# Kernel optimization log

Hardware: AMD Instinct MI355X
Metric: run time of the kernel (lower is better)

Reference implementation:

```python
import jax, jax.numpy as jnp
import numpy as np

# dims: batch, query/key grid HxW, channels, heads (== W for the final matmul to be consistent)
B, H, W, DIM, HEADS = 4, 64, 64, 512, 64
QKV = DIM // HEADS          # per-head projection width (8)
SCALE = QKV ** -0.5         # self.qkv_dim ** -0.5


def setup_inputs() -> dict:
    key = jax.random.key(0)
    k1, k2, k3, k4 = jax.random.split(key, 4)
    x = jax.random.normal(k1, (B, H, W, DIM), dtype=jnp.float32)
    # AttnVector weights, init std=0.01 as in nn.init.normal_(self.w, std=0.01)
    w_q = jax.random.normal(k2, (DIM, HEADS, QKV), dtype=jnp.float32) * 0.01
    w_k = jax.random.normal(k3, (DIM, HEADS, QKV), dtype=jnp.float32) * 0.01
    w_v = jax.random.normal(k4, (DIM, HEADS, QKV), dtype=jnp.float32) * 0.01
    return {"x": x, "w_q": w_q, "w_k": w_k, "w_v": w_v}


def reference(x, w_q, w_k, w_v):
    # q, k, v projections: einsum 'bhwc,cnp->bhwnp' -> [B,H,W,HEADS,QKV]
    q = jnp.einsum('bhwc,cnp->bhwnp', x, w_q)
    k = jnp.einsum('bhwc,cnp->bhwnp', x, w_k)
    v = jnp.einsum('bhwc,cnp->bhwnp', x, w_v)
    # Literal math of torch.einsum('bhwc,bpqd->bhwpq', q, k): the contracted
    # labels c and d appear only once each, so each tensor is summed over its
    # feature axes independently and the result is an outer product over
    # spatial positions: weights[b,h,w,p,q] = sum(q[b,h,w]) * sum(k[b,p,q]).
    qs = q.sum(axis=(-2, -1))  # [B,H,W]
    ks = k.sum(axis=(-2, -1))  # [B,H,W]
    weights = qs[:, :, :, None, None] * ks[:, None, None, :, :]  # [B,H,W,H,W]
    # dropout (p=0.1) is identity in eval mode; scale applied BEFORE softmax,
    # exactly as in the source (weights *= scale; softmax(dim=-1)).
    weights = jax.nn.softmax(weights * SCALE, axis=-1)
    # weights @ value: batch dims (B,H,W), matmul (H_p, W_q) @ (heads==W_q, QKV)
    attn = jnp.einsum('bhwpq,bhwqd->bhwpd', weights, v)  # [B,H,W,H,QKV]
    return attn
```

## Files before the change

kernel.cpp:

```cpp
#include <hip/hip_runtime.h>
#include <hip/hip_bf16.h>
#include <math.h>


#define SCALE 0.35355339059327373f
#define LOG2E 1.4426950408889634f

typedef __attribute__((ext_vector_type(8))) short s16x8;
typedef __attribute__((ext_vector_type(4))) float f32x4;
typedef __attribute__((ext_vector_type(4))) unsigned int u32x4;

union frag_cast { u32x4 u; s16x8 s; };

__device__ __forceinline__ unsigned short f2bf(float f) {
    unsigned u = __float_as_uint(f);
    u += 0x7FFF + ((u >> 16) & 1);
    return (unsigned short)(u >> 16);
}
__device__ __forceinline__ float bf2f(unsigned short h) {
    return __uint_as_float(((unsigned)h) << 16);
}

__device__ __forceinline__ void gl16(const void* g, void* l) {
    __builtin_amdgcn_global_load_lds(
        (const __attribute__((address_space(1))) unsigned int*)g,
        (__attribute__((address_space(3))) unsigned int*)l, 16, 0, 0);
}

__device__ __forceinline__ void split2(float f0, float f1, unsigned& h, unsigned& l) {
    unsigned u0 = __float_as_uint(f0), u1 = __float_as_uint(f1);
    h = __builtin_amdgcn_perm(u1, u0, 0x07060302u);
    float l0 = f0 - __uint_as_float(u0 & 0xffff0000u);
    float l1 = f1 - __uint_as_float(u1 & 0xffff0000u);
    unsigned lp;
    asm("v_cvt_pk_bf16_f32 %0, %1, %2" : "=v"(lp) : "v"(l0), "v"(l1));
    l = lp;
}

__global__ __launch_bounds__(256) void k_prep(const float* __restrict__ wq,
                                              const float* __restrict__ wk,
                                              const float* __restrict__ wv,
                                              float* __restrict__ wqs,
                                              float* __restrict__ wks,
                                              unsigned short* __restrict__ wh,
                                              unsigned short* __restrict__ wl) {
    __shared__ float tile[64][65];
    if (blockIdx.x >= 64) {
        int gw = ((int)blockIdx.x - 64) * 4 + (threadIdx.x >> 6);
        int lane = threadIdx.x & 63;
        const float* src = (gw < 512) ? wq : wk;
        int c = gw & 511;
        const float4* row = (const float4*)(src + (size_t)c * 512);
        float4 a = row[lane * 2], b = row[lane * 2 + 1];
        float s = a.x + a.y + a.z + a.w + b.x + b.y + b.z + b.w;
#pragma unroll
        for (int off = 32; off; off >>= 1) s += __shfl_xor(s, off);
        if (lane == 0) {
            if (gw < 512) wqs[c] = s; else wks[c] = s;
        }
        return;
    }
    const int ti = (int)blockIdx.x >> 3;
    const int tj = (int)blockIdx.x & 7;
    const int r = threadIdx.x >> 4;
    const int c4 = (threadIdx.x & 15) * 4;
#pragma unroll
    for (int i = 0; i < 4; ++i) {
        int kl = r + i * 16;
        float4 v = *(const float4*)(wv + (size_t)(ti * 64 + kl) * 512 + tj * 64 + c4);
        tile[kl][c4 + 0] = v.x; tile[kl][c4 + 1] = v.y;
        tile[kl][c4 + 2] = v.z; tile[kl][c4 + 3] = v.w;
    }
    __syncthreads();
#pragma unroll
    for (int i = 0; i < 4; ++i) {
        int nl = r + i * 16;
        int n = tj * 64 + nl;
        ushort4 h4, l4;
        float v0 = tile[c4 + 0][nl], v1 = tile[c4 + 1][nl];
        float v2 = tile[c4 + 2][nl], v3 = tile[c4 + 3][nl];
        h4.x = f2bf(v0); l4.x = f2bf(v0 - bf2f(h4.x));
        h4.y = f2bf(v1); l4.y = f2bf(v1 - bf2f(h4.y));
        h4.z = f2bf(v2); l4.z = f2bf(v2 - bf2f(h4.z));
        h4.w = f2bf(v3); l4.w = f2bf(v3 - bf2f(h4.w));
        *(ushort4*)(wh + (size_t)n * 512 + ti * 64 + c4) = h4;
        *(ushort4*)(wl + (size_t)n * 512 + ti * 64 + c4) = l4;
    }
}

__global__ __launch_bounds__(256) void k_qsks(const float* __restrict__ x,
                                              const float* __restrict__ wqs,
                                              const float* __restrict__ wks,
                                              float* __restrict__ qs,
                                              float* __restrict__ ks) {
    int row = (int)blockIdx.x * 4 + (threadIdx.x >> 6);
    int lane = threadIdx.x & 63;
    const float4* xr = (const float4*)(x + (size_t)row * 512);
    const float4* q4 = (const float4*)wqs;
    const float4* k4 = (const float4*)wks;
    float sq = 0.f, sk = 0.f;
#pragma unroll
    for (int i = 0; i < 2; ++i) {
        float4 xv = xr[lane * 2 + i];
        float4 qv = q4[lane * 2 + i];
        float4 kv = k4[lane * 2 + i];
        sq += xv.x * qv.x + xv.y * qv.y + xv.z * qv.z + xv.w * qv.w;
        sk += xv.x * kv.x + xv.y * kv.y + xv.z * kv.z + xv.w * kv.w;
    }
#pragma unroll
    for (int off = 32; off; off >>= 1) {
        sq += __shfl_xor(sq, off);
        sk += __shfl_xor(sk, off);
    }
    if (lane == 0) { qs[row] = sq; ks[row] = sk; }
}

__global__ __launch_bounds__(64) void k_prep2(const float* __restrict__ ks,
                                              float* __restrict__ kmax,
                                              float* __restrict__ kmin,
                                              float* __restrict__ L) {
    int bp = blockIdx.x;
    int b = bp >> 6, p = bp & 63;
    int q = threadIdx.x;
    float v = ks[bp * 64 + q];
    float hi = v, lo = v;
#pragma unroll
    for (int off = 32; off; off >>= 1) {
        hi = fmaxf(hi, __shfl_xor(hi, off));
        lo = fminf(lo, __shfl_xor(lo, off));
    }
    if (q == 0) { kmax[bp] = hi; kmin[bp] = lo; }
    L[((b * 64 + q) * 16 + (p & 15)) * 4 + (p >> 4)] = v;
}

__global__ __launch_bounds__(512, 4) void k_vgemm(const float* __restrict__ x,
                                                  const unsigned short* __restrict__ wh,
                                                  const unsigned short* __restrict__ wl,
                                                  float* __restrict__ V) {
    __shared__ float Af[128 * 32];
    __shared__ unsigned short Bhs[128 * 32];
    __shared__ unsigned short Bls[128 * 32];

    const int tid = threadIdx.x;
    const int wave = tid >> 6, lane = tid & 63;
    const int mblk = (int)(blockIdx.x >> 2) * 128;
    const int nblk = (int)(blockIdx.x & 3) * 128;
    const int wm = wave >> 2, wn = wave & 3;
    const int arow = lane & 15, kgrp = lane >> 4;

    const int ar = tid >> 3, ap = tid & 7;
    const float* gA0 = x + (size_t)(mblk + ar) * 512 + (size_t)(((ap ^ (ar & 7)) * 4));
    const float* gA1 = gA0 + (size_t)64 * 512;
    const int br = tid >> 2, bp = tid & 3;
    const size_t boff = (size_t)(nblk + br) * 512 + (size_t)((bp ^ (br & 3)) * 8);
    const unsigned short* gBh = wh + boff;
    const unsigned short* gBl = wl + boff;
    float* lA0 = Af + tid * 4;
    float* lA1 = Af + (tid + 512) * 4;
    unsigned short* lBh = Bhs + tid * 8;
    unsigned short* lBl = Bls + tid * 8;

    f32x4 acc[4][2];
#pragma unroll
    for (int mt = 0; mt < 4; ++mt)
#pragma unroll
        for (int nt = 0; nt < 2; ++nt) acc[mt][nt] = (f32x4){0.f, 0.f, 0.f, 0.f};

    for (int step = 0; step < 16; ++step) {
        gl16(gA0, lA0); gl16(gA1, lA1);
        gl16(gBh, lBh); gl16(gBl, lBl);
        gA0 += 32; gA1 += 32; gBh += 32; gBl += 32;
        __syncthreads();

        s16x8 ah[4], al[4], bh[2], bl[2];
        const int s = arow & 7;
#pragma unroll
        for (int mt = 0; mt < 4; ++mt) {
            const int rowa = wm * 64 + mt * 16 + arow;
            const float* base = Af + rowa * 32;
            f32x4 lo = *(const f32x4*)(base + (((kgrp * 2) ^ s) * 4));
            f32x4 hi = *(const f32x4*)(base + (((kgrp * 2 + 1) ^ s) * 4));
            unsigned h0, h1, h2, h3, l0, l1, l2, l3;
            split2(lo[0], lo[1], h0, l0);
            split2(lo[2], lo[3], h1, l1);
            split2(hi[0], hi[1], h2, l2);
            split2(hi[2], hi[3], h3, l3);
            frag_cast H, L;
            H.u = (u32x4){h0, h1, h2, h3};
            L.u = (u32x4){l0, l1, l2, l3};
            ah[mt] = H.s; al[mt] = L.s;
        }
#pragma unroll
        for (int nt = 0; nt < 2; ++nt) {
            const int rowb = wn * 32 + nt * 16 + arow;
            const int pb = kgrp ^ (rowb & 3);
            bh[nt] = *(const s16x8*)(Bhs + rowb * 32 + pb * 8);
            bl[nt] = *(const s16x8*)(Bls + rowb * 32 + pb * 8);
        }
#pragma unroll
        for (int mt = 0; mt < 4; ++mt)
#pragma unroll
            for (int nt = 0; nt < 2; ++nt) {
                acc[mt][nt] = __builtin_amdgcn_mfma_f32_16x16x32_bf16(ah[mt], bh[nt], acc[mt][nt], 0, 0, 0);
                acc[mt][nt] = __builtin_amdgcn_mfma_f32_16x16x32_bf16(al[mt], bh[nt], acc[mt][nt], 0, 0, 0);
                acc[mt][nt] = __builtin_amdgcn_mfma_f32_16x16x32_bf16(ah[mt], bl[nt], acc[mt][nt], 0, 0, 0);
            }
        __syncthreads();
    }

    const int rbase = (lane >> 4) * 4;
#pragma unroll
    for (int mt = 0; mt < 4; ++mt)
#pragma unroll
        for (int nt = 0; nt < 2; ++nt) {
            const int col = nblk + wn * 32 + nt * 16 + arow;
#pragma unroll
            for (int r = 0; r < 4; ++r) {
                const int row = mblk + wm * 64 + mt * 16 + rbase + r;
                V[(size_t)row * 512 + col] = acc[mt][nt][r];
            }
        }
}

__global__ __launch_bounds__(256) void k_attn(float* __restrict__ io,
                                              const float* __restrict__ qs,
                                              const float* __restrict__ L,
                                              const float* __restrict__ kmax,
                                              const float* __restrict__ kmin) {
    __shared__ float vsm[16 * 520];
    __shared__ float Lsm[4096];
    const int tid = threadIdx.x;
    const int r0 = (int)blockIdx.x * 16;
    const int b = r0 >> 12;

    {
        const float4* vg = (const float4*)(io + (size_t)r0 * 512);
#pragma unroll
        for (int i = 0; i < 8; ++i) {
            int idx4 = tid + 256 * i;
            *(float4*)(vsm + (idx4 >> 7) * 520 + (idx4 & 127) * 4) = vg[idx4];
        }
        const float4* Lg = (const float4*)(L + (size_t)b * 4096);
#pragma unroll
        for (int i = 0; i < 4; ++i)
            *(float4*)(Lsm + (tid + 256 * i) * 4) = Lg[tid + 256 * i];
    }
    __syncthreads();

    const int m = tid >> 4, p0 = tid & 15;
    const float t2 = qs[r0 + m] * (SCALE * LOG2E);
    float rm2[4], den[4], acc[4][8];
#pragma unroll
    for (int j = 0; j < 4; ++j) {
        float khi = kmax[b * 64 + p0 + 16 * j];
        float klo = kmin[b * 64 + p0 + 16 * j];
        rm2[j] = (t2 >= 0.f) ? t2 * khi : t2 * klo;
        den[j] = 0.f;
#pragma unroll
        for (int d = 0; d < 8; ++d) acc[j][d] = 0.f;
    }
    const float* vrow = vsm + m * 520;
#pragma unroll 4
    for (int q = 0; q < 64; ++q) {
        const float4 kv = *(const float4*)(Lsm + (q * 16 + p0) * 4);
        const f32x4 v0 = *(const f32x4*)(vrow + q * 8);
        const f32x4 v1 = *(const f32x4*)(vrow + q * 8 + 4);
        const float kvj[4] = {kv.x, kv.y, kv.z, kv.w};
#pragma unroll
        for (int j = 0; j < 4; ++j) {
            const float e = exp2f(fmaf(t2, kvj[j], -rm2[j]));
            den[j] += e;
            acc[j][0] = fmaf(e, v0[0], acc[j][0]);
            acc[j][1] = fmaf(e, v0[1], acc[j][1]);
            acc[j][2] = fmaf(e, v0[2], acc[j][2]);
            acc[j][3] = fmaf(e, v0[3], acc[j][3]);
            acc[j][4] = fmaf(e, v1[0], acc[j][4]);
            acc[j][5] = fmaf(e, v1[1], acc[j][5]);
            acc[j][6] = fmaf(e, v1[2], acc[j][6]);
            acc[j][7] = fmaf(e, v1[3], acc[j][7]);
        }
    }
#pragma unroll
    for (int j = 0; j < 4; ++j) {
        const float inv = 1.0f / den[j];
        float4* o = (float4*)(io + (size_t)(r0 + m) * 512 + (p0 + 16 * j) * 8);
        o[0] = make_float4(acc[j][0] * inv, acc[j][1] * inv, acc[j][2] * inv, acc[j][3] * inv);
        o[1] = make_float4(acc[j][4] * inv, acc[j][5] * inv, acc[j][6] * inv, acc[j][7] * inv);
    }
}

extern "C" void kernel_launch(void* const* d_in, const int* in_sizes, int n_in,
                              void* d_out, int out_size, void* d_ws, size_t ws_size,
                              hipStream_t stream) {
    const float* x  = (const float*)d_in[0];
    const float* wq = (const float*)d_in[1];
    const float* wk = (const float*)d_in[2];
    const float* wv = (const float*)d_in[3];
    float* out = (float*)d_out;

    float* ws   = (float*)d_ws;
    float* qs   = ws;
    float* ks   = ws + 16384;
    float* wqs  = ws + 32768;
    float* wks  = ws + 33280;
    float* kmax = ws + 33792;
    float* kmin = ws + 34048;
    float* L    = ws + 34304;
    unsigned short* wvT_h = (unsigned short*)(ws + 50688);
    unsigned short* wvT_l = wvT_h + 262144;

    hipLaunchKernelGGL(k_prep,  dim3(320),  dim3(256), 0, stream, wq, wk, wv, wqs, wks, wvT_h, wvT_l);
    hipLaunchKernelGGL(k_qsks,  dim3(4096), dim3(256), 0, stream, x, wqs, wks, qs, ks);
    hipLaunchKernelGGL(k_prep2, dim3(256),  dim3(64),  0, stream, ks, kmax, kmin, L);
    hipLaunchKernelGGL(k_vgemm, dim3(512),  dim3(512), 0, stream, x, wvT_h, wvT_l, out);
    hipLaunchKernelGGL(k_attn,  dim3(1024), dim3(256), 0, stream, out, qs, L, kmax, kmin);
}
```

Before: 152.9 us.

## Replace split-bf16 V projection GEMM with single-pass fp16 MFMA

Drops the three-MFMA split-bf16 emulation of fp32 in the V projection. Instead, x is converted to fp16 inside the qs/ks kernel and the weights are stored as fp16, so the GEMM issues one f16 MFMA per tile. The GEMM also changes shape: 256 threads per block, 64-deep K steps with 8 iterations, and 4x4 accumulator tiles per wave. This cuts MFMA work, LDS traffic and conversion ALU work, but lowers precision to fp16 and adds an extra write and read of x in fp16.

```diff
diff --git a/kernel.cpp b/kernel.cpp
--- a/kernel.cpp
+++ b/kernel.cpp
@@ -6,35 +6,14 @@
 #define SCALE 0.35355339059327373f
 #define LOG2E 1.4426950408889634f
 
-typedef __attribute__((ext_vector_type(8))) short s16x8;
+typedef __attribute__((ext_vector_type(8))) _Float16 f16x8;
+typedef __attribute__((ext_vector_type(4))) _Float16 f16x4;
 typedef __attribute__((ext_vector_type(4))) float f32x4;
-typedef __attribute__((ext_vector_type(4))) unsigned int u32x4;
-
-union frag_cast { u32x4 u; s16x8 s; };
-
-__device__ __forceinline__ unsigned short f2bf(float f) {
-    unsigned u = __float_as_uint(f);
-    u += 0x7FFF + ((u >> 16) & 1);
-    return (unsigned short)(u >> 16);
-}
-__device__ __forceinline__ float bf2f(unsigned short h) {
-    return __uint_as_float(((unsigned)h) << 16);
-}
 
 __device__ __forceinline__ void gl16(const void* g, void* l) {
     __builtin_amdgcn_global_load_lds(
         (const __attribute__((address_space(1))) unsigned int*)g,
         (__attribute__((address_space(3))) unsigned int*)l, 16, 0, 0);
-}
-
-__device__ __forceinline__ void split2(float f0, float f1, unsigned& h, unsigned& l) {
-    unsigned u0 = __float_as_uint(f0), u1 = __float_as_uint(f1);
-    h = __builtin_amdgcn_perm(u1, u0, 0x07060302u);
-    float l0 = f0 - __uint_as_float(u0 & 0xffff0000u);
-    float l1 = f1 - __uint_as_float(u1 & 0xffff0000u);
-    unsigned lp;
-    asm("v_cvt_pk_bf16_f32 %0, %1, %2" : "=v"(lp) : "v"(l0), "v"(l1));
-    l = lp;
 }
 
 __global__ __launch_bounds__(256) void k_prep(const float* __restrict__ wq,
@@ -42,8 +21,7 @@
                                               const float* __restrict__ wv,
                                               float* __restrict__ wqs,
                                               float* __restrict__ wks,
-                                              unsigned short* __restrict__ wh,
-                                              unsigned short* __restrict__ wl) {
+                                              _Float16* __restrict__ whf) {
     __shared__ float tile[64][65];
     if (blockIdx.x >= 64) {
         int gw = ((int)blockIdx.x - 64) * 4 + (threadIdx.x >> 6);
@@ -76,15 +54,12 @@
     for (int i = 0; i < 4; ++i) {
         int nl = r + i * 16;
         int n = tj * 64 + nl;
-        ushort4 h4, l4;
-        float v0 = tile[c4 + 0][nl], v1 = tile[c4 + 1][nl];
-        float v2 = tile[c4 + 2][nl], v3 = tile[c4 + 3][nl];
-        h4.x = f2bf(v0); l4.x = f2bf(v0 - bf2f(h4.x));
-        h4.y = f2bf(v1); l4.y = f2bf(v1 - bf2f(h4.y));
-        h4.z = f2bf(v2); l4.z = f2bf(v2 - bf2f(h4.z));
-        h4.w = f2bf(v3); l4.w = f2bf(v3 - bf2f(h4.w));
-        *(ushort4*)(wh + (size_t)n * 512 + ti * 64 + c4) = h4;
-        *(ushort4*)(wl + (size_t)n * 512 + ti * 64 + c4) = l4;
+        f16x4 h4;
+        h4[0] = (_Float16)tile[c4 + 0][nl];
+        h4[1] = (_Float16)tile[c4 + 1][nl];
+        h4[2] = (_Float16)tile[c4 + 2][nl];
+        h4[3] = (_Float16)tile[c4 + 3][nl];
+        *(f16x4*)(whf + (size_t)n * 512 + ti * 64 + c4) = h4;
     }
 }
 
@@ -92,21 +67,26 @@
                                               const float* __restrict__ wqs,
                                               const float* __restrict__ wks,
                                               float* __restrict__ qs,
-                                              float* __restrict__ ks) {
+                                              float* __restrict__ ks,
+                                              _Float16* __restrict__ xh) {
     int row = (int)blockIdx.x * 4 + (threadIdx.x >> 6);
     int lane = threadIdx.x & 63;
     const float4* xr = (const float4*)(x + (size_t)row * 512);
     const float4* q4 = (const float4*)wqs;
     const float4* k4 = (const float4*)wks;
-    float sq = 0.f, sk = 0.f;
-#pragma unroll
-    for (int i = 0; i < 2; ++i) {
-        float4 xv = xr[lane * 2 + i];
-        float4 qv = q4[lane * 2 + i];
-        float4 kv = k4[lane * 2 + i];
-        sq += xv.x * qv.x + xv.y * qv.y + xv.z * qv.z + xv.w * qv.w;
-        sk += xv.x * kv.x + xv.y * kv.y + xv.z * kv.z + xv.w * kv.w;
-    }
+    float4 xv0 = xr[lane * 2], xv1 = xr[lane * 2 + 1];
+    float4 qv0 = q4[lane * 2], qv1 = q4[lane * 2 + 1];
+    float4 kv0 = k4[lane * 2], kv1 = k4[lane * 2 + 1];
+    float sq = xv0.x * qv0.x + xv0.y * qv0.y + xv0.z * qv0.z + xv0.w * qv0.w
+             + xv1.x * qv1.x + xv1.y * qv1.y + xv1.z * qv1.z + xv1.w * qv1.w;
+    float sk = xv0.x * kv0.x + xv0.y * kv0.y + xv0.z * kv0.z + xv0.w * kv0.w
+             + xv1.x * kv1.x + xv1.y * kv1.y + xv1.z * kv1.z + xv1.w * kv1.w;
+    f16x8 hv;
+    hv[0] = (_Float16)xv0.x; hv[1] = (_Float16)xv0.y;
+    hv[2] = (_Float16)xv0.z; hv[3] = (_Float16)xv0.w;
+    hv[4] = (_Float16)xv1.x; hv[5] = (_Float16)xv1.y;
+    hv[6] = (_Float16)xv1.z; hv[7] = (_Float16)xv1.w;
+    *(f16x8*)(xh + (size_t)row * 512 + lane * 8) = hv;
 #pragma unroll
     for (int off = 32; off; off >>= 1) {
         sq += __shfl_xor(sq, off);
@@ -133,78 +113,64 @@
     L[((b * 64 + q) * 16 + (p & 15)) * 4 + (p >> 4)] = v;
 }
 
-__global__ __launch_bounds__(512, 4) void k_vgemm(const float* __restrict__ x,
-                                                  const unsigned short* __restrict__ wh,
-                                                  const unsigned short* __restrict__ wl,
+__global__ __launch_bounds__(256, 3) void k_vgemm(const _Float16* __restrict__ xh,
+                                                  const _Float16* __restrict__ whf,
                                                   float* __restrict__ V) {
-    __shared__ float Af[128 * 32];
-    __shared__ unsigned short Bhs[128 * 32];
-    __shared__ unsigned short Bls[128 * 32];
+    __shared__ _Float16 As[128 * 64];
+    __shared__ _Float16 Bs[128 * 64];
 
     const int tid = threadIdx.x;
     const int wave = tid >> 6, lane = tid & 63;
     const int mblk = (int)(blockIdx.x >> 2) * 128;
     const int nblk = (int)(blockIdx.x & 3) * 128;
-    const int wm = wave >> 2, wn = wave & 3;
+    const int wm = wave >> 1, wn = wave & 1;
     const int arow = lane & 15, kgrp = lane >> 4;
-
-    const int ar = tid >> 3, ap = tid & 7;
-    const float* gA0 = x + (size_t)(mblk + ar) * 512 + (size_t)(((ap ^ (ar & 7)) * 4));
-    const float* gA1 = gA0 + (size_t)64 * 512;
-    const int br = tid >> 2, bp = tid & 3;
-    const size_t boff = (size_t)(nblk + br) * 512 + (size_t)((bp ^ (br & 3)) * 8);
-    const unsigned short* gBh = wh + boff;
-    const unsigned short* gBl = wl + boff;
-    float* lA0 = Af + tid * 4;
-    float* lA1 = Af + (tid + 512) * 4;
-    unsigned short* lBh = Bhs + tid * 8;
-    unsigned short* lBl = Bls + tid * 8;
-
-    f32x4 acc[4][2];
+    const int s7 = arow & 7;
+
+    const _Float16* pa[4]; const _Float16* pb[4];
+    _Float16* la[4]; _Float16* lb[4];
+#pragma unroll
+    for (int i = 0; i < 4; ++i) {
+        const int g = i * 256 + tid;
+        const int row = g >> 3, gp = g & 7;
+        const int gs = (gp ^ (row & 7)) * 8;
+        pa[i] = xh + (size_t)(mblk + row) * 512 + gs;
+        pb[i] = whf + (size_t)(nblk + row) * 512 + gs;
+        la[i] = As + g * 8;
+        lb[i] = Bs + g * 8;
+    }
+
+    f32x4 acc[4][4];
 #pragma unroll
     for (int mt = 0; mt < 4; ++mt)
 #pragma unroll
-        for (int nt = 0; nt < 2; ++nt) acc[mt][nt] = (f32x4){0.f, 0.f, 0.f, 0.f};
-
-    for (int step = 0; step < 16; ++step) {
-        gl16(gA0, lA0); gl16(gA1, lA1);
-        gl16(gBh, lBh); gl16(gBl, lBl);
-        gA0 += 32; gA1 += 32; gBh += 32; gBl += 32;
+        for (int nt = 0; nt < 4; ++nt) acc[mt][nt] = (f32x4){0.f, 0.f, 0.f, 0.f};
+
+    for (int step = 0; step < 8; ++step) {
+#pragma unroll
+        for (int i = 0; i < 4; ++i) gl16(pa[i], la[i]);
+#pragma unroll
+        for (int i = 0; i < 4; ++i) gl16(pb[i], lb[i]);
+#pragma unroll
+        for (int i = 0; i < 4; ++i) { pa[i] += 64; pb[i] += 64; }
         __syncthreads();
 
-        s16x8 ah[4], al[4], bh[2], bl[2];
-        const int s = arow & 7;
-#pragma unroll
-        for (int mt = 0; mt < 4; ++mt) {
-            const int rowa = wm * 64 + mt * 16 + arow;
-            const float* base = Af + rowa * 32;
-            f32x4 lo = *(const f32x4*)(base + (((kgrp * 2) ^ s) * 4));
-            f32x4 hi = *(const f32x4*)(base + (((kgrp * 2 + 1) ^ s) * 4));
-            unsigned h0, h1, h2, h3, l0, l1, l2, l3;
-            split2(lo[0], lo[1], h0, l0);
-            split2(lo[2], lo[3], h1, l1);
-            split2(hi[0], hi[1], h2, l2);
-            split2(hi[2], hi[3], h3, l3);
-            frag_cast H, L;
-            H.u = (u32x4){h0, h1, h2, h3};
-            L.u = (u32x4){l0, l1, l2, l3};
-            ah[mt] = H.s; al[mt] = L.s;
-        }
-#pragma unroll
-        for (int nt = 0; nt < 2; ++nt) {
-            const int rowb = wn * 32 + nt * 16 + arow;
-            const int pb = kgrp ^ (rowb & 3);
-            bh[nt] = *(const s16x8*)(Bhs + rowb * 32 + pb * 8);
-            bl[nt] = *(const s16x8*)(Bls + rowb * 32 + pb * 8);
-        }
-#pragma unroll
-        for (int mt = 0; mt < 4; ++mt)
-#pragma unroll
-            for (int nt = 0; nt < 2; ++nt) {
-                acc[mt][nt] = __builtin_amdgcn_mfma_f32_16x16x32_bf16(ah[mt], bh[nt], acc[mt][nt], 0, 0, 0);
-                acc[mt][nt] = __builtin_amdgcn_mfma_f32_16x16x32_bf16(al[mt], bh[nt], acc[mt][nt], 0, 0, 0);
-                acc[mt][nt] = __builtin_amdgcn_mfma_f32_16x16x32_bf16(ah[mt], bl[nt], acc[mt][nt], 0, 0, 0);
-            }
+#pragma unroll
+        for (int sub = 0; sub < 2; ++sub) {
+            f16x8 a[4], b[4];
+            const int pg = ((sub * 4 + kgrp) ^ s7) * 8;
+#pragma unroll
+            for (int mt = 0; mt < 4; ++mt)
+                a[mt] = *(const f16x8*)(As + (wm * 64 + mt * 16 + arow) * 64 + pg);
+#pragma unroll
+            for (int nt = 0; nt < 4; ++nt)
+                b[nt] = *(const f16x8*)(Bs + (wn * 64 + nt * 16 + arow) * 64 + pg);
+#pragma unroll
+            for (int mt = 0; mt < 4; ++mt)
+#pragma unroll
+                for (int nt = 0; nt < 4; ++nt)
+                    acc[mt][nt] = __builtin_amdgcn_mfma_f32_16x16x32_f16(a[mt], b[nt], acc[mt][nt], 0, 0, 0);
+        }
         __syncthreads();
     }
 
@@ -212,8 +178,8 @@
 #pragma unroll
     for (int mt = 0; mt < 4; ++mt)
 #pragma unroll
-        for (int nt = 0; nt < 2; ++nt) {
-            const int col = nblk + wn * 32 + nt * 16 + arow;
+        for (int nt = 0; nt < 4; ++nt) {
+            const int col = nblk + wn * 64 + nt * 16 + arow;
 #pragma unroll
             for (int r = 0; r < 4; ++r) {
                 const int row = mblk + wm * 64 + mt * 16 + rbase + r;
@@ -306,12 +272,12 @@
     float* kmax = ws + 33792;
     float* kmin = ws + 34048;
     float* L    = ws + 34304;
-    unsigned short* wvT_h = (unsigned short*)(ws + 50688);
-    unsigned short* wvT_l = wvT_h + 262144;
-
-    hipLaunchKernelGGL(k_prep,  dim3(320),  dim3(256), 0, stream, wq, wk, wv, wqs, wks, wvT_h, wvT_l);
-    hipLaunchKernelGGL(k_qsks,  dim3(4096), dim3(256), 0, stream, x, wqs, wks, qs, ks);
+    _Float16* whf = (_Float16*)(ws + 50688);
+    _Float16* xh  = (_Float16*)(ws + 181760);
+
+    hipLaunchKernelGGL(k_prep,  dim3(320),  dim3(256), 0, stream, wq, wk, wv, wqs, wks, whf);
+    hipLaunchKernelGGL(k_qsks,  dim3(4096), dim3(256), 0, stream, x, wqs, wks, qs, ks, xh);
     hipLaunchKernelGGL(k_prep2, dim3(256),  dim3(64),  0, stream, ks, kmax, kmin, L);
-    hipLaunchKernelGGL(k_vgemm, dim3(512),  dim3(512), 0, stream, x, wvT_h, wvT_l, out);
+    hipLaunchKernelGGL(k_vgemm, dim3(512),  dim3(256), 0, stream, xh, whf, out);
     hipLaunchKernelGGL(k_attn,  dim3(1024), dim3(256), 0, stream, out, qs, L, kmax, kmin);
 }
```

After: 140.0 us. -8.4%, faster.
